# Optimization experiments

Hardware: AMD Instinct MI355X
Metric: run time of the kernel (lower is better)

## Reference

```python
import jax, jax.numpy as jnp
import numpy as np

B, L, D = 1, 2048, 2048
NH, NKV, HD = 32, 8, 64          # heads, kv heads, head_dim = D // NH
THETA = 50000.0
EPS = 1e-5
SCALE = HD ** -0.5


def _rope(x):
    # traditional (interleaved-pair) RoPE; x: (B, H, L, HD)
    hd = x.shape[-1]
    pos = jnp.arange(x.shape[2], dtype=jnp.float32)
    inv = THETA ** (-jnp.arange(0, hd, 2, dtype=jnp.float32) / hd)
    ang = pos[:, None] * inv[None, :]              # (L, HD/2)
    cos, sin = jnp.cos(ang), jnp.sin(ang)
    x1, x2 = x[..., ::2], x[..., 1::2]
    r1 = x1 * cos - x2 * sin
    r2 = x1 * sin + x2 * cos
    return jnp.stack([r1, r2], axis=-1).reshape(x.shape)


def _rmsnorm(x, w):
    return x * jax.lax.rsqrt(jnp.mean(x * x, axis=-1, keepdims=True) + EPS) * w


def setup_inputs() -> dict:
    key = jax.random.key(0)
    ks = jax.random.split(key, 5)
    x = jax.random.normal(ks[0], (B, L, D), dtype=jnp.float32)
    w_qkv = jax.random.normal(ks[1], (NH * HD + 2 * NKV * HD, D), dtype=jnp.float32) * 0.02
    w_out = jax.random.normal(ks[2], (D, D), dtype=jnp.float32) * 0.02
    q_gamma = 1.0 + 0.02 * jax.random.normal(ks[3], (HD,), dtype=jnp.float32)
    k_gamma = 1.0 + 0.02 * jax.random.normal(ks[4], (HD,), dtype=jnp.float32)
    mask = jnp.tril(jnp.ones((L, L), dtype=bool))   # causal
    return {"x": x, "w_qkv": w_qkv, "w_out": w_out,
            "q_gamma": q_gamma, "k_gamma": k_gamma, "mask": mask}


def reference(x, w_qkv, w_out, q_gamma, k_gamma, mask):
    b, l, d = x.shape
    qkv = x @ w_qkv.T                               # fused QKV proj (no bias)
    q, k, v = jnp.split(qkv, [NH * HD, NH * HD + NKV * HD], axis=-1)
    q = q.reshape(b, l, NH, HD).transpose(0, 2, 1, 3)     # (B,NH,L,HD)
    k = k.reshape(b, l, NKV, HD).transpose(0, 2, 1, 3)    # (B,NKV,L,HD)
    v = v.reshape(b, l, NKV, HD).transpose(0, 2, 1, 3)
    q = _rmsnorm(_rope(q), q_gamma)
    k = _rmsnorm(_rope(k), k_gamma)
    g = NH // NKV                                   # GQA group size
    qg = q.reshape(b, NKV, g, l, HD)
    scores = jnp.einsum('bkgqd,bkld->bkgql', qg, k) * SCALE
    scores = jnp.where(mask, scores, -jnp.inf)
    attn = jax.nn.softmax(scores, axis=-1)
    out = jnp.einsum('bkgql,bkld->bkgqd', attn, v)  # (B,NKV,g,L,HD)
    out = out.reshape(b, NH, l, HD).transpose(0, 2, 1, 3).reshape(b, l, d)
    return out @ w_out.T
```

## Files before the change

kernel.cpp:

```cpp
#include <hip/hip_runtime.h>

using bf16   = __bf16;
using bf16x4 = __bf16 __attribute__((ext_vector_type(4)));
using bf16x8 = __bf16 __attribute__((ext_vector_type(8)));
using f32x4  = float __attribute__((ext_vector_type(4)));
using f32x16 = float __attribute__((ext_vector_type(16)));
using u32x2  = unsigned int __attribute__((ext_vector_type(2)));
using u32x4  = unsigned int __attribute__((ext_vector_type(4)));

#define L_SEQ  2048
#define DMODEL 2048
#define NQH    32
#define NKVH   8
#define HDIM   64
#define QKV_N  3072

#define KVF_HSTRIDE (64 * 4 * 64 * 8)

__device__ __forceinline__ void gload_lds16(const void* g, void* lds) {
  __builtin_amdgcn_global_load_lds((__attribute__((address_space(1))) void*)(g),
                                   (__attribute__((address_space(3))) void*)(lds),
                                   16, 0, 0);
}

__device__ __forceinline__ unsigned pack2(float a, float b) {
  union { bf16 h[2]; unsigned u; } x;
  x.h[0] = (bf16)a; x.h[1] = (bf16)b;
  return x.u;
}

__device__ __forceinline__ bf16x8 make_pfrag(float p0, float p1, float p2, float p3,
                                             float p4, float p5, float p6, float p7,
                                             int hi) {
  const unsigned W0 = pack2(p0, p1);
  const unsigned W1 = pack2(p2, p3);
  const unsigned W2 = pack2(p4, p5);
  const unsigned W3 = pack2(p6, p7);
  u32x4 pw;
#if __has_builtin(__builtin_amdgcn_permlane32_swap)
  {
    using i32x2 = int __attribute__((ext_vector_type(2)));
    const i32x2 r02 = __builtin_amdgcn_permlane32_swap((int)W0, (int)W2, false, false);
    const i32x2 r13 = __builtin_amdgcn_permlane32_swap((int)W1, (int)W3, false, false);
    pw = u32x4{ (unsigned)r02[0], (unsigned)r13[0], (unsigned)r02[1], (unsigned)r13[1] };
  }
#else
  {
    const unsigned X0 = (unsigned)__shfl_xor((int)W0, 32);
    const unsigned X1 = (unsigned)__shfl_xor((int)W1, 32);
    const unsigned X2 = (unsigned)__shfl_xor((int)W2, 32);
    const unsigned X3 = (unsigned)__shfl_xor((int)W3, 32);
    pw = u32x4{ hi ? X2 : W0, hi ? X3 : W1, hi ? W2 : X0, hi ? W3 : X1 };
  }
#endif
  return __builtin_bit_cast(bf16x8, pw);
}

__device__ __forceinline__ int chunk_base64(int Qb) {
  return (Qb < 8)  ? Qb
       : (Qb < 16) ? 8  + 2 * (Qb - 8)
       : (Qb < 24) ? 24 + 3 * (Qb - 16)
                   : 48 + 4 * (Qb - 24);
}

#define N4_X  (L_SEQ * DMODEL / 4)
#define N4_WQ (QKV_N * DMODEL / 4)
#define N4_WO (DMODEL * DMODEL / 4)
__global__ void cvt3_f32_bf16(const float* __restrict__ x, const float* __restrict__ wq,
                              const float* __restrict__ wo, bf16* __restrict__ xb,
                              bf16* __restrict__ wqb, bf16* __restrict__ wob) {
  const long stride = (long)gridDim.x * blockDim.x;
  const long ntot = N4_X + N4_WQ + N4_WO;
  for (long i = (long)blockIdx.x * blockDim.x + threadIdx.x; i < ntot; i += stride) {
    const float* src; bf16* dst; long j;
    if (i < N4_X)               { src = x;  dst = xb;  j = i; }
    else if (i < N4_X + N4_WQ)  { src = wq; dst = wqb; j = i - N4_X; }
    else                        { src = wo; dst = wob; j = i - N4_X - N4_WQ; }
    const float4 v = reinterpret_cast<const float4*>(src)[j];
    bf16x4 o = { (bf16)v.x, (bf16)v.y, (bf16)v.z, (bf16)v.w };
    reinterpret_cast<bf16x4*>(dst)[j] = o;
  }
}

template <typename OutT>
__global__ __launch_bounds__(128)
void gemm_bt(const bf16* __restrict__ A, const bf16* __restrict__ B,
             OutT* __restrict__ C, int M, int N, int K) {
  __shared__ bf16 As[128 * 64];
  __shared__ bf16 Bs[64 * 64];
  const int tid = threadIdx.x;
  const int w = tid >> 6, l = tid & 63;
  const int lq = l & 15, lg = l >> 4;
  const long m0 = (long)blockIdx.y * 128;
  const long n0 = (long)blockIdx.x * 64;
  const int ks = K / gridDim.z;
  const int kb = blockIdx.z * ks;
  C += (long)blockIdx.z * M * N;

  const int lrow = l >> 3;
  const int scol = ((l & 7) ^ lrow) << 3;

  f32x4 acc[4][4];
#pragma unroll
  for (int i = 0; i < 4; ++i)
#pragma unroll
    for (int j = 0; j < 4; ++j) acc[i][j] = f32x4{0.f, 0.f, 0.f, 0.f};

  for (int k0 = kb; k0 < kb + ks; k0 += 64) {
#pragma unroll
    for (int i = 0; i < 8; ++i) {
      const int r0 = (i * 2 + w) * 8;
      gload_lds16(A + (m0 + r0 + lrow) * (long)K + k0 + scol, &As[r0 * 64]);
    }
#pragma unroll
    for (int i = 0; i < 4; ++i) {
      const int r0 = (i * 2 + w) * 8;
      gload_lds16(B + (n0 + r0 + lrow) * (long)K + k0 + scol, &Bs[r0 * 64]);
    }
    __syncthreads();
#pragma unroll
    for (int kk = 0; kk < 2; ++kk) {
      bf16x8 af[4], bfr[4];
#pragma unroll
      for (int t = 0; t < 4; ++t) {
        const int rowA = w * 64 + t * 16 + lq;
        const int blkA = (kk * 4 + lg) ^ (rowA & 7);
        af[t] = *reinterpret_cast<const bf16x8*>(&As[rowA * 64 + blkA * 8]);
        const int rowB = t * 16 + lq;
        const int blkB = (kk * 4 + lg) ^ (rowB & 7);
        bfr[t] = *reinterpret_cast<const bf16x8*>(&Bs[rowB * 64 + blkB * 8]);
      }
#pragma unroll
      for (int mt = 0; mt < 4; ++mt)
#pragma unroll
        for (int nt = 0; nt < 4; ++nt)
          acc[mt][nt] = __builtin_amdgcn_mfma_f32_16x16x32_bf16(af[mt], bfr[nt], acc[mt][nt], 0, 0, 0);
    }
    __syncthreads();
  }

#pragma unroll
  for (int mt = 0; mt < 4; ++mt)
#pragma unroll
    for (int r = 0; r < 4; ++r) {
      const long row = m0 + w * 64 + mt * 16 + lg * 4 + r;
#pragma unroll
      for (int nt = 0; nt < 4; ++nt) {
        const long col = n0 + nt * 16 + lq;
        C[row * (long)N + col] = (OutT)acc[mt][nt][r];
      }
    }
}

__global__ __launch_bounds__(256)
void rope_rms(const bf16* __restrict__ pA, const bf16* __restrict__ pB,
              const float* __restrict__ qg, const float* __restrict__ kg,
              bf16* __restrict__ qo, bf16* __restrict__ kfr) {
  const int gid = blockIdx.x * 4 + (threadIdx.x >> 6);
  const int lane = threadIdx.x & 63;
  const int pos = gid / 40;
  const int hh = gid % 40;
  const bool isq = hh < 32;
  const int col = isq ? hh * HDIM : NQH * HDIM + (hh - 32) * HDIM;

  const long idx = (long)pos * QKV_N + col + lane;
  float x = (float)pA[idx] + (float)pB[idx];
  float p = __shfl_xor(x, 1);
  const float fi = (float)(lane & ~1) * (1.0f / 64.0f);
  const float inv = powf(50000.0f, -fi);
  const float ang = (float)pos * inv;
  const float sn = sinf(ang), cs = cosf(ang);
  const float r = (lane & 1) ? (p * sn + x * cs) : (x * cs - p * sn);

  float ss = r * r;
#pragma unroll
  for (int off = 1; off < 64; off <<= 1) ss += __shfl_xor(ss, off);
  const float scl = rsqrtf(ss * (1.0f / 64.0f) + 1e-5f);
  const float g = isq ? qg[lane] : kg[lane];
  const float o = r * scl * g;

  if (isq) {
    qo[(long)pos * DMODEL + hh * HDIM + lane] = (bf16)(o * 0.18033688011112042f);
  } else {
    const int kvh = hh - 32;
    const int d = lane;
    const int lp = (pos & 31) + (((d >> 3) & 1) << 5);
    const long kidx = ((((long)kvh * 64 + (pos >> 5)) * 4 + (d >> 4)) * 64 + lp) * 8 + (d & 7);
    kfr[kidx] = (bf16)o;
  }
}

__global__ __launch_bounds__(256)
void repack_v(const bf16* __restrict__ pA, const bf16* __restrict__ pB,
              bf16* __restrict__ vfr) {
  __shared__ bf16 t[32][72];
  const int kvh = blockIdx.x >> 6;
  const int kb = blockIdx.x & 63;
  const int tid = threadIdx.x;

  {
    const int row = tid >> 3;
    const int cc = (tid & 7) * 8;
    const long goff = (long)(kb * 32 + row) * QKV_N + (NQH * HDIM + NKVH * HDIM) + kvh * HDIM + cc;
    const bf16x8 a = *reinterpret_cast<const bf16x8*>(pA + goff);
    const bf16x8 b = *reinterpret_cast<const bf16x8*>(pB + goff);
    bf16x8 s;
#pragma unroll
    for (int e = 0; e < 8; ++e) s[e] = (bf16)((float)a[e] + (float)b[e]);
    *reinterpret_cast<bf16x8*>(&t[row][cc]) = s;
  }
  __syncthreads();

  const int f = tid >> 6, l = tid & 63;
  const int s = f >> 1, dh = f & 1;
  const int hi = l >> 5, l31 = l & 31;
  union { bf16 b[8]; u32x4 u; } o;
#pragma unroll
  for (int e = 0; e < 8; ++e) o.b[e] = t[s * 16 + hi * 8 + e][dh * 32 + l31];
  bf16* od = vfr + (((long)(kvh * 64 + kb) * 4 + f) * 64 + l) * 8;
  *reinterpret_cast<u32x4*>(od) = o.u;
}

__global__ __launch_bounds__(256, 2)
void flash_attn(const bf16* __restrict__ Q, const bf16* __restrict__ Kfr,
                const bf16* __restrict__ Vfr,
                bf16* __restrict__ po, float* __restrict__ pm, float* __restrict__ pl) {
  const int w = threadIdx.x >> 6, l = threadIdx.x & 63;
  const int lane31 = l & 31, hi = l >> 5;
  const int bb = blockIdx.x;
  const int kvh = bb & 7;
  const int g = 79 - (bb >> 3);

  int Qb, c;
  if (g < 8)       { Qb = g;                   c = 0; }
  else if (g < 24) { Qb = 8 + ((g - 8) >> 1);  c = (g - 8) & 1; }
  else if (g < 48) { Qb = 16 + (g - 24) / 3;   c = (g - 24) % 3; }
  else             { Qb = 24 + ((g - 48) >> 2); c = (g - 48) & 3; }

  const int h = kvh * 4 + w;
  const int s0 = c * 16;
  const int s1 = min(2 * Qb + 2, s0 + 16);
  const int pidx = h * 80 + g;

  const int q0A = Qb * 64;
  const int qA = q0A + lane31;
  const int qB = q0A + 32 + lane31;
  const int l8 = l * 8;

  const bf16* kfrh = Kfr + (long)kvh * KVF_HSTRIDE;
  const bf16* vfrh = Vfr + (long)kvh * KVF_HSTRIDE;

  const bf16* qrowA = Q + (long)qA * DMODEL + h * HDIM + hi * 8;
  const bf16* qrowB = Q + (long)qB * DMODEL + h * HDIM + hi * 8;
  bf16x8 qfA[4], qfB[4];
#pragma unroll
  for (int cc = 0; cc < 4; ++cc) {
    qfA[cc] = *reinterpret_cast<const bf16x8*>(qrowA + cc * 16);
    qfB[cc] = *reinterpret_cast<const bf16x8*>(qrowB + cc * 16);
  }

  f32x16 oA0, oA1, oB0, oB1;
#pragma unroll
  for (int r = 0; r < 16; ++r) { oA0[r] = 0.f; oA1[r] = 0.f; oB0[r] = 0.f; oB1[r] = 0.f; }
  float mA = -3.0e38f, lsA = 0.f, mB = -3.0e38f, lsB = 0.f;

  bf16x8 kc0, kc1, kc2, kc3;
  {
    const bf16* kp = kfrh + (long)s0 * 2048 + l8;
    kc0 = *reinterpret_cast<const bf16x8*>(kp);
    kc1 = *reinterpret_cast<const bf16x8*>(kp + 512);
    kc2 = *reinterpret_cast<const bf16x8*>(kp + 1024);
    kc3 = *reinterpret_cast<const bf16x8*>(kp + 1536);
  }

  for (int sti = s0; sti < s1; ++sti) {
    const int kb0 = sti * 32;

    const bf16* vp = vfrh + (long)sti * 2048 + l8;
    const bf16x8 va0 = *reinterpret_cast<const bf16x8*>(vp);
    const bf16x8 vb0 = *reinterpret_cast<const bf16x8*>(vp + 512);
    const bf16x8 va1 = *reinterpret_cast<const bf16x8*>(vp + 1024);
    const bf16x8 vb1 = *reinterpret_cast<const bf16x8*>(vp + 1536);

    const long knoff = (sti + 1 < s1) ? (long)(sti + 1) * 2048 : (long)s0 * 2048;
    const bf16* kp = kfrh + knoff + l8;
    const bf16x8 kn0 = *reinterpret_cast<const bf16x8*>(kp);
    const bf16x8 kn1 = *reinterpret_cast<const bf16x8*>(kp + 512);
    const bf16x8 kn2 = *reinterpret_cast<const bf16x8*>(kp + 1024);
    const bf16x8 kn3 = *reinterpret_cast<const bf16x8*>(kp + 1536);

    if (kb0 <= q0A + 31) {
      f32x16 st;
#pragma unroll
      for (int r = 0; r < 16; ++r) st[r] = 0.f;
      st = __builtin_amdgcn_mfma_f32_32x32x16_bf16(kc0, qfA[0], st, 0, 0, 0);
      st = __builtin_amdgcn_mfma_f32_32x32x16_bf16(kc1, qfA[1], st, 0, 0, 0);
      st = __builtin_amdgcn_mfma_f32_32x32x16_bf16(kc2, qfA[2], st, 0, 0, 0);
      st = __builtin_amdgcn_mfma_f32_32x32x16_bf16(kc3, qfA[3], st, 0, 0, 0);

      if (kb0 + 31 > q0A) {
#pragma unroll
        for (int r = 0; r < 16; ++r) {
          const int k_abs = kb0 + (r & 3) + 8 * (r >> 2) + 4 * hi;
          if (k_abs > qA) st[r] = -3.0e38f;
        }
      }

      float t[8];
#pragma unroll
      for (int r = 0; r < 8; ++r) t[r] = fmaxf(st[r], st[r + 8]);
#pragma unroll
      for (int s = 4; s > 0; s >>= 1)
#pragma unroll
        for (int r = 0; r < 4; ++r) if (r < s) t[r] = fmaxf(t[r], t[r + s]);
      const float mx = fmaxf(t[0], __shfl_xor(t[0], 32));

      if (!__all(mx - mA <= 8.0f)) {
        const float mn = fmaxf(mA, mx);
        const float al = __builtin_amdgcn_exp2f(mA - mn);
        mA = mn; lsA *= al;
#pragma unroll
        for (int r = 0; r < 16; ++r) { oA0[r] *= al; oA1[r] *= al; }
      }
      float rs = 0.f;
#pragma unroll
      for (int r = 0; r < 16; ++r) { st[r] = __builtin_amdgcn_exp2f(st[r] - mA); rs += st[r]; }
      rs += __shfl_xor(rs, 32);
      lsA += rs;

      const bf16x8 pf0 = make_pfrag(st[0], st[1], st[2], st[3], st[4], st[5], st[6], st[7], hi);
      oA0 = __builtin_amdgcn_mfma_f32_32x32x16_bf16(va0, pf0, oA0, 0, 0, 0);
      oA1 = __builtin_amdgcn_mfma_f32_32x32x16_bf16(vb0, pf0, oA1, 0, 0, 0);
      const bf16x8 pf1 = make_pfrag(st[8], st[9], st[10], st[11], st[12], st[13], st[14], st[15], hi);
      oA0 = __builtin_amdgcn_mfma_f32_32x32x16_bf16(va1, pf1, oA0, 0, 0, 0);
      oA1 = __builtin_amdgcn_mfma_f32_32x32x16_bf16(vb1, pf1, oA1, 0, 0, 0);
    }

    {
      f32x16 st;
#pragma unroll
      for (int r = 0; r < 16; ++r) st[r] = 0.f;
      st = __builtin_amdgcn_mfma_f32_32x32x16_bf16(kc0, qfB[0], st, 0, 0, 0);
      st = __builtin_amdgcn_mfma_f32_32x32x16_bf16(kc1, qfB[1], st, 0, 0, 0);
      st = __builtin_amdgcn_mfma_f32_32x32x16_bf16(kc2, qfB[2], st, 0, 0, 0);
      st = __builtin_amdgcn_mfma_f32_32x32x16_bf16(kc3, qfB[3], st, 0, 0, 0);

      if (kb0 + 31 > q0A + 32) {
#pragma unroll
        for (int r = 0; r < 16; ++r) {
          const int k_abs = kb0 + (r & 3) + 8 * (r >> 2) + 4 * hi;
          if (k_abs > qB) st[r] = -3.0e38f;
        }
      }

      float t[8];
#pragma unroll
      for (int r = 0; r < 8; ++r) t[r] = fmaxf(st[r], st[r + 8]);
#pragma unroll
      for (int s = 4; s > 0; s >>= 1)
#pragma unroll
        for (int r = 0; r < 4; ++r) if (r < s) t[r] = fmaxf(t[r], t[r + s]);
      const float mx = fmaxf(t[0], __shfl_xor(t[0], 32));

      if (!__all(mx - mB <= 8.0f)) {
        const float mn = fmaxf(mB, mx);
        const float al = __builtin_amdgcn_exp2f(mB - mn);
        mB = mn; lsB *= al;
#pragma unroll
        for (int r = 0; r < 16; ++r) { oB0[r] *= al; oB1[r] *= al; }
      }
      float rs = 0.f;
#pragma unroll
      for (int r = 0; r < 16; ++r) { st[r] = __builtin_amdgcn_exp2f(st[r] - mB); rs += st[r]; }
      rs += __shfl_xor(rs, 32);
      lsB += rs;

      const bf16x8 pf0 = make_pfrag(st[0], st[1], st[2], st[3], st[4], st[5], st[6], st[7], hi);
      oB0 = __builtin_amdgcn_mfma_f32_32x32x16_bf16(va0, pf0, oB0, 0, 0, 0);
      oB1 = __builtin_amdgcn_mfma_f32_32x32x16_bf16(vb0, pf0, oB1, 0, 0, 0);
      const bf16x8 pf1 = make_pfrag(st[8], st[9], st[10], st[11], st[12], st[13], st[14], st[15], hi);
      oB0 = __builtin_amdgcn_mfma_f32_32x32x16_bf16(va1, pf1, oB0, 0, 0, 0);
      oB1 = __builtin_amdgcn_mfma_f32_32x32x16_bf16(vb1, pf1, oB1, 0, 0, 0);
    }

    kc0 = kn0; kc1 = kn1; kc2 = kn2; kc3 = kn3;
  }

  bf16* pbase = po + (long)pidx * 4096;
#pragma unroll
  for (int gg = 0; gg < 4; ++gg) {
    const int d0 = 8 * gg + 4 * hi;
    u32x2 a0 = { pack2(oA0[4 * gg + 0], oA0[4 * gg + 1]),
                 pack2(oA0[4 * gg + 2], oA0[4 * gg + 3]) };
    u32x2 a1 = { pack2(oA1[4 * gg + 0], oA1[4 * gg + 1]),
                 pack2(oA1[4 * gg + 2], oA1[4 * gg + 3]) };
    *reinterpret_cast<u32x2*>(pbase + lane31 * 64 + d0) = a0;
    *reinterpret_cast<u32x2*>(pbase + lane31 * 64 + 32 + d0) = a1;
    u32x2 b0 = { pack2(oB0[4 * gg + 0], oB0[4 * gg + 1]),
                 pack2(oB0[4 * gg + 2], oB0[4 * gg + 3]) };
    u32x2 b1 = { pack2(oB1[4 * gg + 0], oB1[4 * gg + 1]),
                 pack2(oB1[4 * gg + 2], oB1[4 * gg + 3]) };
    *reinterpret_cast<u32x2*>(pbase + (32 + lane31) * 64 + d0) = b0;
    *reinterpret_cast<u32x2*>(pbase + (32 + lane31) * 64 + 32 + d0) = b1;
  }
  if (hi == 0) {
    pm[pidx * 64 + lane31] = mA;
    pl[pidx * 64 + lane31] = lsA;
    pm[pidx * 64 + 32 + lane31] = mB;
    pl[pidx * 64 + 32 + lane31] = lsB;
  }
}

__global__ __launch_bounds__(256)
void combine_split(const bf16* __restrict__ po, const float* __restrict__ pm,
                   const float* __restrict__ pl, bf16* __restrict__ ao) {
  const int t = blockIdx.x;
  const int tid = threadIdx.x;
  const int r = tid >> 2;
  const int dc = (tid & 3) * 16;
  const int h = t >> 5, Qb = t & 31;
  const int nc = (Qb < 8) ? 1 : (Qb < 16) ? 2 : (Qb < 24) ? 3 : 4;
  const int p0 = h * 80 + chunk_base64(Qb);

  float mv0 = -3e38f, mv1 = -3e38f, mv2 = -3e38f, mv3 = -3e38f;
  float lv0 = 0.f, lv1 = 0.f, lv2 = 0.f, lv3 = 0.f;
  mv0 = pm[(p0 + 0) * 64 + r];              lv0 = pl[(p0 + 0) * 64 + r];
  if (nc > 1) { mv1 = pm[(p0 + 1) * 64 + r]; lv1 = pl[(p0 + 1) * 64 + r]; }
  if (nc > 2) { mv2 = pm[(p0 + 2) * 64 + r]; lv2 = pl[(p0 + 2) * 64 + r]; }
  if (nc > 3) { mv3 = pm[(p0 + 3) * 64 + r]; lv3 = pl[(p0 + 3) * 64 + r]; }
  const float M = fmaxf(fmaxf(mv0, mv1), fmaxf(mv2, mv3));
  const float w0 = __builtin_amdgcn_exp2f(mv0 - M);
  const float w1 = (nc > 1) ? __builtin_amdgcn_exp2f(mv1 - M) : 0.f;
  const float w2 = (nc > 2) ? __builtin_amdgcn_exp2f(mv2 - M) : 0.f;
  const float w3 = (nc > 3) ? __builtin_amdgcn_exp2f(mv3 - M) : 0.f;
  const float invL = 1.0f / (lv0 * w0 + lv1 * w1 + lv2 * w2 + lv3 * w3);

  float acc[16];
#pragma unroll
  for (int j = 0; j < 16; ++j) acc[j] = 0.f;

#pragma unroll
  for (int c = 0; c < 4; ++c) {
    if (c < nc) {
      const float fc = ((c == 0) ? w0 : (c == 1) ? w1 : (c == 2) ? w2 : w3) * invL;
      const bf16* src = po + ((long)(p0 + c) * 4096) + r * 64 + dc;
      const bf16x8 a0 = *reinterpret_cast<const bf16x8*>(src);
      const bf16x8 a1 = *reinterpret_cast<const bf16x8*>(src + 8);
#pragma unroll
      for (int j = 0; j < 8; ++j) {
        acc[j]     += (float)a0[j] * fc;
        acc[8 + j] += (float)a1[j] * fc;
      }
    }
  }

  const long q_abs = (long)Qb * 64 + r;
  bf16* od = ao + q_abs * DMODEL + h * HDIM + dc;
  union { bf16 b[16]; u32x4 u[2]; } o;
#pragma unroll
  for (int j = 0; j < 16; ++j) o.b[j] = (bf16)acc[j];
  *reinterpret_cast<u32x4*>(od) = o.u[0];
  *reinterpret_cast<u32x4*>(od + 8) = o.u[1];
}

extern "C" void kernel_launch(void* const* d_in, const int* in_sizes, int n_in,
                              void* d_out, int out_size, void* d_ws, size_t ws_size,
                              hipStream_t stream) {
  const float* x       = (const float*)d_in[0];
  const float* w_qkv   = (const float*)d_in[1];
  const float* w_out   = (const float*)d_in[2];
  const float* q_gamma = (const float*)d_in[3];
  const float* k_gamma = (const float*)d_in[4];

  char* ws = (char*)d_ws;
  bf16* xb    = (bf16*)(ws);
  bf16* wqb   = (bf16*)(ws + (8ul  << 20));
  bf16* wob   = (bf16*)(ws + (20ul << 20));
  bf16* qkvpA = (bf16*)(ws + (28ul << 20));
  bf16* qkvpB = (bf16*)(ws + (40ul << 20));
  bf16* qb    = (bf16*)(ws);
  bf16* kfr   = (bf16*)(ws + (8ul  << 20));
  bf16* vfr   = (bf16*)(ws + (10ul << 20));
  bf16* po    = (bf16*)(ws + (28ul << 20));
  float* pm   = (float*)(ws + (48ul << 20));
  float* pl   = (float*)(ws + (49ul << 20));
  bf16* ao    = (bf16*)(ws + (52ul << 20));
  float* out  = (float*)d_out;

  cvt3_f32_bf16<<<2048, 256, 0, stream>>>(x, w_qkv, w_out, xb, wqb, wob);

  gemm_bt<bf16><<<dim3(QKV_N / 64, L_SEQ / 128, 2), 128, 0, stream>>>(xb, wqb, qkvpA, L_SEQ, QKV_N, DMODEL);

  rope_rms<<<(L_SEQ * 40) / 4, 256, 0, stream>>>(qkvpA, qkvpB, q_gamma, k_gamma, qb, kfr);
  repack_v<<<NKVH * (L_SEQ / 32), 256, 0, stream>>>(qkvpA, qkvpB, vfr);

  flash_attn<<<640, 256, 0, stream>>>(qb, kfr, vfr, po, pm, pl);
  combine_split<<<1024, 256, 0, stream>>>(po, pm, pl, ao);

  gemm_bt<float><<<dim3(DMODEL / 64, L_SEQ / 128, 1), 128, 0, stream>>>(ao, wob, out, L_SEQ, DMODEL, DMODEL);
}
```

Baseline: 171.6 us.

## Use fixed softmax offset, drop online max, fuse rope/V repack kernels

Replaces the running-max online softmax in flash attention with a constant exponent offset. This is justified by the RMS-normalised Q and K keeping scores bounded, so the per-tile max reduction, rescaling and the stored max values go away. Split-KV combining becomes a plain sum of partial outputs and row sums. Single-chunk query blocks now write normalised output directly, so combine only runs on multi-chunk blocks. The rope/RMS and V repack kernels are merged into one launch. The risk is overflow or underflow if the gamma weights make scores exceed the assumed bound.

Result: faster. 162.5 us (median of 2 runs) (-5.3%).

```diff
diff --git a/kernel.cpp b/kernel.cpp
--- a/kernel.cpp
+++ b/kernel.cpp
@@ -16,6 +16,8 @@
 #define QKV_N  3072
 
 #define KVF_HSTRIDE (64 * 4 * 64 * 8)
+
+#define FIXED_M 16.0f
 
 __device__ __forceinline__ void gload_lds16(const void* g, void* lds) {
   __builtin_amdgcn_global_load_lds((__attribute__((address_space(1))) void*)(g),
@@ -153,78 +155,76 @@
 }
 
 __global__ __launch_bounds__(256)
-void rope_rms(const bf16* __restrict__ pA, const bf16* __restrict__ pB,
-              const float* __restrict__ qg, const float* __restrict__ kg,
-              bf16* __restrict__ qo, bf16* __restrict__ kfr) {
-  const int gid = blockIdx.x * 4 + (threadIdx.x >> 6);
-  const int lane = threadIdx.x & 63;
-  const int pos = gid / 40;
-  const int hh = gid % 40;
-  const bool isq = hh < 32;
-  const int col = isq ? hh * HDIM : NQH * HDIM + (hh - 32) * HDIM;
-
-  const long idx = (long)pos * QKV_N + col + lane;
-  float x = (float)pA[idx] + (float)pB[idx];
-  float p = __shfl_xor(x, 1);
-  const float fi = (float)(lane & ~1) * (1.0f / 64.0f);
-  const float inv = powf(50000.0f, -fi);
-  const float ang = (float)pos * inv;
-  const float sn = sinf(ang), cs = cosf(ang);
-  const float r = (lane & 1) ? (p * sn + x * cs) : (x * cs - p * sn);
-
-  float ss = r * r;
-#pragma unroll
-  for (int off = 1; off < 64; off <<= 1) ss += __shfl_xor(ss, off);
-  const float scl = rsqrtf(ss * (1.0f / 64.0f) + 1e-5f);
-  const float g = isq ? qg[lane] : kg[lane];
-  const float o = r * scl * g;
-
-  if (isq) {
-    qo[(long)pos * DMODEL + hh * HDIM + lane] = (bf16)(o * 0.18033688011112042f);
+void rope_repack(const bf16* __restrict__ pA, const bf16* __restrict__ pB,
+                 const float* __restrict__ qg, const float* __restrict__ kg,
+                 bf16* __restrict__ qo, bf16* __restrict__ kfr, bf16* __restrict__ vfr) {
+  __shared__ bf16 t[32][72];
+  if (blockIdx.x < 20480) {
+    const int gid = blockIdx.x * 4 + (threadIdx.x >> 6);
+    const int lane = threadIdx.x & 63;
+    const int pos = gid / 40;
+    const int hh = gid % 40;
+    const bool isq = hh < 32;
+    const int col = isq ? hh * HDIM : NQH * HDIM + (hh - 32) * HDIM;
+
+    const long idx = (long)pos * QKV_N + col + lane;
+    float x = (float)pA[idx] + (float)pB[idx];
+    float p = __shfl_xor(x, 1);
+    const float fi = (float)(lane & ~1) * (1.0f / 64.0f);
+    const float inv = powf(50000.0f, -fi);
+    const float ang = (float)pos * inv;
+    const float sn = sinf(ang), cs = cosf(ang);
+    const float r = (lane & 1) ? (p * sn + x * cs) : (x * cs - p * sn);
+
+    float ss = r * r;
+#pragma unroll
+    for (int off = 1; off < 64; off <<= 1) ss += __shfl_xor(ss, off);
+    const float scl = rsqrtf(ss * (1.0f / 64.0f) + 1e-5f);
+    const float g = isq ? qg[lane] : kg[lane];
+    const float o = r * scl * g;
+
+    if (isq) {
+      qo[(long)pos * DMODEL + hh * HDIM + lane] = (bf16)(o * 0.18033688011112042f);
+    } else {
+      const int kvh = hh - 32;
+      const int d = lane;
+      const int lp = (pos & 31) + (((d >> 3) & 1) << 5);
+      const long kidx = ((((long)kvh * 64 + (pos >> 5)) * 4 + (d >> 4)) * 64 + lp) * 8 + (d & 7);
+      kfr[kidx] = (bf16)o;
+    }
   } else {
-    const int kvh = hh - 32;
-    const int d = lane;
-    const int lp = (pos & 31) + (((d >> 3) & 1) << 5);
-    const long kidx = ((((long)kvh * 64 + (pos >> 5)) * 4 + (d >> 4)) * 64 + lp) * 8 + (d & 7);
-    kfr[kidx] = (bf16)o;
-  }
-}
-
-__global__ __launch_bounds__(256)
-void repack_v(const bf16* __restrict__ pA, const bf16* __restrict__ pB,
-              bf16* __restrict__ vfr) {
-  __shared__ bf16 t[32][72];
-  const int kvh = blockIdx.x >> 6;
-  const int kb = blockIdx.x & 63;
-  const int tid = threadIdx.x;
-
-  {
-    const int row = tid >> 3;
-    const int cc = (tid & 7) * 8;
-    const long goff = (long)(kb * 32 + row) * QKV_N + (NQH * HDIM + NKVH * HDIM) + kvh * HDIM + cc;
-    const bf16x8 a = *reinterpret_cast<const bf16x8*>(pA + goff);
-    const bf16x8 b = *reinterpret_cast<const bf16x8*>(pB + goff);
-    bf16x8 s;
-#pragma unroll
-    for (int e = 0; e < 8; ++e) s[e] = (bf16)((float)a[e] + (float)b[e]);
-    *reinterpret_cast<bf16x8*>(&t[row][cc]) = s;
-  }
-  __syncthreads();
-
-  const int f = tid >> 6, l = tid & 63;
-  const int s = f >> 1, dh = f & 1;
-  const int hi = l >> 5, l31 = l & 31;
-  union { bf16 b[8]; u32x4 u; } o;
-#pragma unroll
-  for (int e = 0; e < 8; ++e) o.b[e] = t[s * 16 + hi * 8 + e][dh * 32 + l31];
-  bf16* od = vfr + (((long)(kvh * 64 + kb) * 4 + f) * 64 + l) * 8;
-  *reinterpret_cast<u32x4*>(od) = o.u;
+    const int bid = blockIdx.x - 20480;
+    const int kvh = bid >> 6;
+    const int kb = bid & 63;
+    const int tid = threadIdx.x;
+    {
+      const int row = tid >> 3;
+      const int cc = (tid & 7) * 8;
+      const long goff = (long)(kb * 32 + row) * QKV_N + (NQH * HDIM + NKVH * HDIM) + kvh * HDIM + cc;
+      const bf16x8 a = *reinterpret_cast<const bf16x8*>(pA + goff);
+      const bf16x8 b = *reinterpret_cast<const bf16x8*>(pB + goff);
+      bf16x8 s;
+#pragma unroll
+      for (int e = 0; e < 8; ++e) s[e] = (bf16)((float)a[e] + (float)b[e]);
+      *reinterpret_cast<bf16x8*>(&t[row][cc]) = s;
+    }
+    __syncthreads();
+
+    const int f = tid >> 6, l = tid & 63;
+    const int s = f >> 1, dh = f & 1;
+    const int hi = l >> 5, l31 = l & 31;
+    union { bf16 b[8]; u32x4 u; } o;
+#pragma unroll
+    for (int e = 0; e < 8; ++e) o.b[e] = t[s * 16 + hi * 8 + e][dh * 32 + l31];
+    bf16* od = vfr + (((long)(kvh * 64 + kb) * 4 + f) * 64 + l) * 8;
+    *reinterpret_cast<u32x4*>(od) = o.u;
+  }
 }
 
 __global__ __launch_bounds__(256, 2)
 void flash_attn(const bf16* __restrict__ Q, const bf16* __restrict__ Kfr,
                 const bf16* __restrict__ Vfr,
-                bf16* __restrict__ po, float* __restrict__ pm, float* __restrict__ pl) {
+                bf16* __restrict__ po, float* __restrict__ pl, bf16* __restrict__ ao) {
   const int w = threadIdx.x >> 6, l = threadIdx.x & 63;
   const int lane31 = l & 31, hi = l >> 5;
   const int bb = blockIdx.x;
@@ -262,7 +262,7 @@
   f32x16 oA0, oA1, oB0, oB1;
 #pragma unroll
   for (int r = 0; r < 16; ++r) { oA0[r] = 0.f; oA1[r] = 0.f; oB0[r] = 0.f; oB1[r] = 0.f; }
-  float mA = -3.0e38f, lsA = 0.f, mB = -3.0e38f, lsB = 0.f;
+  float lsA = 0.f, lsB = 0.f;
 
   bf16x8 kc0, kc1, kc2, kc3;
   {
@@ -306,25 +306,9 @@
         }
       }
 
-      float t[8];
-#pragma unroll
-      for (int r = 0; r < 8; ++r) t[r] = fmaxf(st[r], st[r + 8]);
-#pragma unroll
-      for (int s = 4; s > 0; s >>= 1)
-#pragma unroll
-        for (int r = 0; r < 4; ++r) if (r < s) t[r] = fmaxf(t[r], t[r + s]);
-      const float mx = fmaxf(t[0], __shfl_xor(t[0], 32));
-
-      if (!__all(mx - mA <= 8.0f)) {
-        const float mn = fmaxf(mA, mx);
-        const float al = __builtin_amdgcn_exp2f(mA - mn);
-        mA = mn; lsA *= al;
-#pragma unroll
-        for (int r = 0; r < 16; ++r) { oA0[r] *= al; oA1[r] *= al; }
-      }
       float rs = 0.f;
 #pragma unroll
-      for (int r = 0; r < 16; ++r) { st[r] = __builtin_amdgcn_exp2f(st[r] - mA); rs += st[r]; }
+      for (int r = 0; r < 16; ++r) { st[r] = __builtin_amdgcn_exp2f(st[r] - FIXED_M); rs += st[r]; }
       rs += __shfl_xor(rs, 32);
       lsA += rs;
 
@@ -353,25 +337,9 @@
         }
       }
 
-      float t[8];
-#pragma unroll
-      for (int r = 0; r < 8; ++r) t[r] = fmaxf(st[r], st[r + 8]);
-#pragma unroll
-      for (int s = 4; s > 0; s >>= 1)
-#pragma unroll
-        for (int r = 0; r < 4; ++r) if (r < s) t[r] = fmaxf(t[r], t[r + s]);
-      const float mx = fmaxf(t[0], __shfl_xor(t[0], 32));
-
-      if (!__all(mx - mB <= 8.0f)) {
-        const float mn = fmaxf(mB, mx);
-        const float al = __builtin_amdgcn_exp2f(mB - mn);
-        mB = mn; lsB *= al;
-#pragma unroll
-        for (int r = 0; r < 16; ++r) { oB0[r] *= al; oB1[r] *= al; }
-      }
       float rs = 0.f;
 #pragma unroll
-      for (int r = 0; r < 16; ++r) { st[r] = __builtin_amdgcn_exp2f(st[r] - mB); rs += st[r]; }
+      for (int r = 0; r < 16; ++r) { st[r] = __builtin_amdgcn_exp2f(st[r] - FIXED_M); rs += st[r]; }
       rs += __shfl_xor(rs, 32);
       lsB += rs;
 
@@ -386,54 +354,67 @@
     kc0 = kn0; kc1 = kn1; kc2 = kn2; kc3 = kn3;
   }
 
-  bf16* pbase = po + (long)pidx * 4096;
-#pragma unroll
-  for (int gg = 0; gg < 4; ++gg) {
-    const int d0 = 8 * gg + 4 * hi;
-    u32x2 a0 = { pack2(oA0[4 * gg + 0], oA0[4 * gg + 1]),
-                 pack2(oA0[4 * gg + 2], oA0[4 * gg + 3]) };
-    u32x2 a1 = { pack2(oA1[4 * gg + 0], oA1[4 * gg + 1]),
-                 pack2(oA1[4 * gg + 2], oA1[4 * gg + 3]) };
-    *reinterpret_cast<u32x2*>(pbase + lane31 * 64 + d0) = a0;
-    *reinterpret_cast<u32x2*>(pbase + lane31 * 64 + 32 + d0) = a1;
-    u32x2 b0 = { pack2(oB0[4 * gg + 0], oB0[4 * gg + 1]),
-                 pack2(oB0[4 * gg + 2], oB0[4 * gg + 3]) };
-    u32x2 b1 = { pack2(oB1[4 * gg + 0], oB1[4 * gg + 1]),
-                 pack2(oB1[4 * gg + 2], oB1[4 * gg + 3]) };
-    *reinterpret_cast<u32x2*>(pbase + (32 + lane31) * 64 + d0) = b0;
-    *reinterpret_cast<u32x2*>(pbase + (32 + lane31) * 64 + 32 + d0) = b1;
-  }
-  if (hi == 0) {
-    pm[pidx * 64 + lane31] = mA;
-    pl[pidx * 64 + lane31] = lsA;
-    pm[pidx * 64 + 32 + lane31] = mB;
-    pl[pidx * 64 + 32 + lane31] = lsB;
+  if (g < 8) {
+    const float rlA = 1.0f / lsA, rlB = 1.0f / lsB;
+    bf16* orowA = ao + (long)qA * DMODEL + h * HDIM;
+    bf16* orowB = ao + (long)qB * DMODEL + h * HDIM;
+#pragma unroll
+    for (int gg = 0; gg < 4; ++gg) {
+      const int d0 = 8 * gg + 4 * hi;
+      u32x2 a0 = { pack2(oA0[4 * gg + 0] * rlA, oA0[4 * gg + 1] * rlA),
+                   pack2(oA0[4 * gg + 2] * rlA, oA0[4 * gg + 3] * rlA) };
+      u32x2 a1 = { pack2(oA1[4 * gg + 0] * rlA, oA1[4 * gg + 1] * rlA),
+                   pack2(oA1[4 * gg + 2] * rlA, oA1[4 * gg + 3] * rlA) };
+      *reinterpret_cast<u32x2*>(orowA + d0) = a0;
+      *reinterpret_cast<u32x2*>(orowA + 32 + d0) = a1;
+      u32x2 b0 = { pack2(oB0[4 * gg + 0] * rlB, oB0[4 * gg + 1] * rlB),
+                   pack2(oB0[4 * gg + 2] * rlB, oB0[4 * gg + 3] * rlB) };
+      u32x2 b1 = { pack2(oB1[4 * gg + 0] * rlB, oB1[4 * gg + 1] * rlB),
+                   pack2(oB1[4 * gg + 2] * rlB, oB1[4 * gg + 3] * rlB) };
+      *reinterpret_cast<u32x2*>(orowB + d0) = b0;
+      *reinterpret_cast<u32x2*>(orowB + 32 + d0) = b1;
+    }
+  } else {
+    bf16* pbase = po + (long)pidx * 4096;
+#pragma unroll
+    for (int gg = 0; gg < 4; ++gg) {
+      const int d0 = 8 * gg + 4 * hi;
+      u32x2 a0 = { pack2(oA0[4 * gg + 0], oA0[4 * gg + 1]),
+                   pack2(oA0[4 * gg + 2], oA0[4 * gg + 3]) };
+      u32x2 a1 = { pack2(oA1[4 * gg + 0], oA1[4 * gg + 1]),
+                   pack2(oA1[4 * gg + 2], oA1[4 * gg + 3]) };
+      *reinterpret_cast<u32x2*>(pbase + lane31 * 64 + d0) = a0;
+      *reinterpret_cast<u32x2*>(pbase + lane31 * 64 + 32 + d0) = a1;
+      u32x2 b0 = { pack2(oB0[4 * gg + 0], oB0[4 * gg + 1]),
+                   pack2(oB0[4 * gg + 2], oB0[4 * gg + 3]) };
+      u32x2 b1 = { pack2(oB1[4 * gg + 0], oB1[4 * gg + 1]),
+                   pack2(oB1[4 * gg + 2], oB1[4 * gg + 3]) };
+      *reinterpret_cast<u32x2*>(pbase + (32 + lane31) * 64 + d0) = b0;
+      *reinterpret_cast<u32x2*>(pbase + (32 + lane31) * 64 + 32 + d0) = b1;
+    }
+    if (hi == 0) {
+      pl[pidx * 64 + lane31] = lsA;
+      pl[pidx * 64 + 32 + lane31] = lsB;
+    }
   }
 }
 
 __global__ __launch_bounds__(256)
-void combine_split(const bf16* __restrict__ po, const float* __restrict__ pm,
-                   const float* __restrict__ pl, bf16* __restrict__ ao) {
+void combine_split(const bf16* __restrict__ po, const float* __restrict__ pl,
+                   bf16* __restrict__ ao) {
   const int t = blockIdx.x;
   const int tid = threadIdx.x;
   const int r = tid >> 2;
   const int dc = (tid & 3) * 16;
-  const int h = t >> 5, Qb = t & 31;
-  const int nc = (Qb < 8) ? 1 : (Qb < 16) ? 2 : (Qb < 24) ? 3 : 4;
+  const int h = t / 24;
+  const int Qb = 8 + (t % 24);
+  const int nc = (Qb < 16) ? 2 : (Qb < 24) ? 3 : 4;
   const int p0 = h * 80 + chunk_base64(Qb);
 
-  float mv0 = -3e38f, mv1 = -3e38f, mv2 = -3e38f, mv3 = -3e38f;
-  float lv0 = 0.f, lv1 = 0.f, lv2 = 0.f, lv3 = 0.f;
-  mv0 = pm[(p0 + 0) * 64 + r];              lv0 = pl[(p0 + 0) * 64 + r];
-  if (nc > 1) { mv1 = pm[(p0 + 1) * 64 + r]; lv1 = pl[(p0 + 1) * 64 + r]; }
-  if (nc > 2) { mv2 = pm[(p0 + 2) * 64 + r]; lv2 = pl[(p0 + 2) * 64 + r]; }
-  if (nc > 3) { mv3 = pm[(p0 + 3) * 64 + r]; lv3 = pl[(p0 + 3) * 64 + r]; }
-  const float M = fmaxf(fmaxf(mv0, mv1), fmaxf(mv2, mv3));
-  const float w0 = __builtin_amdgcn_exp2f(mv0 - M);
-  const float w1 = (nc > 1) ? __builtin_amdgcn_exp2f(mv1 - M) : 0.f;
-  const float w2 = (nc > 2) ? __builtin_amdgcn_exp2f(mv2 - M) : 0.f;
-  const float w3 = (nc > 3) ? __builtin_amdgcn_exp2f(mv3 - M) : 0.f;
-  const float invL = 1.0f / (lv0 * w0 + lv1 * w1 + lv2 * w2 + lv3 * w3);
+  float lv = pl[(p0 + 0) * 64 + r] + pl[(p0 + 1) * 64 + r];
+  if (nc > 2) lv += pl[(p0 + 2) * 64 + r];
+  if (nc > 3) lv += pl[(p0 + 3) * 64 + r];
+  const float invL = 1.0f / lv;
 
   float acc[16];
 #pragma unroll
@@ -442,14 +423,13 @@
 #pragma unroll
   for (int c = 0; c < 4; ++c) {
     if (c < nc) {
-      const float fc = ((c == 0) ? w0 : (c == 1) ? w1 : (c == 2) ? w2 : w3) * invL;
       const bf16* src = po + ((long)(p0 + c) * 4096) + r * 64 + dc;
       const bf16x8 a0 = *reinterpret_cast<const bf16x8*>(src);
       const bf16x8 a1 = *reinterpret_cast<const bf16x8*>(src + 8);
 #pragma unroll
       for (int j = 0; j < 8; ++j) {
-        acc[j]     += (float)a0[j] * fc;
-        acc[8 + j] += (float)a1[j] * fc;
+        acc[j]     += (float)a0[j];
+        acc[8 + j] += (float)a1[j];
       }
     }
   }
@@ -458,7 +438,7 @@
   bf16* od = ao + q_abs * DMODEL + h * HDIM + dc;
   union { bf16 b[16]; u32x4 u[2]; } o;
 #pragma unroll
-  for (int j = 0; j < 16; ++j) o.b[j] = (bf16)acc[j];
+  for (int j = 0; j < 16; ++j) o.b[j] = (bf16)(acc[j] * invL);
   *reinterpret_cast<u32x4*>(od) = o.u[0];
   *reinterpret_cast<u32x4*>(od + 8) = o.u[1];
 }
@@ -482,8 +462,7 @@
   bf16* kfr   = (bf16*)(ws + (8ul  << 20));
   bf16* vfr   = (bf16*)(ws + (10ul << 20));
   bf16* po    = (bf16*)(ws + (28ul << 20));
-  float* pm   = (float*)(ws + (48ul << 20));
-  float* pl   = (float*)(ws + (49ul << 20));
+  float* pl   = (float*)(ws + (48ul << 20));
   bf16* ao    = (bf16*)(ws + (52ul << 20));
   float* out  = (float*)d_out;
 
@@ -491,11 +470,10 @@
 
   gemm_bt<bf16><<<dim3(QKV_N / 64, L_SEQ / 128, 2), 128, 0, stream>>>(xb, wqb, qkvpA, L_SEQ, QKV_N, DMODEL);
 
-  rope_rms<<<(L_SEQ * 40) / 4, 256, 0, stream>>>(qkvpA, qkvpB, q_gamma, k_gamma, qb, kfr);
-  repack_v<<<NKVH * (L_SEQ / 32), 256, 0, stream>>>(qkvpA, qkvpB, vfr);
-
-  flash_attn<<<640, 256, 0, stream>>>(qb, kfr, vfr, po, pm, pl);
-  combine_split<<<1024, 256, 0, stream>>>(po, pm, pl, ao);
+  rope_repack<<<20992, 256, 0, stream>>>(qkvpA, qkvpB, q_gamma, k_gamma, qb, kfr, vfr);
+
+  flash_attn<<<640, 256, 0, stream>>>(qb, kfr, vfr, po, pl, ao);
+  combine_split<<<768, 256, 0, stream>>>(po, pl, ao);
 
   gemm_bt<float><<<dim3(DMODEL / 64, L_SEQ / 128, 1), 128, 0, stream>>>(ao, wob, out, L_SEQ, DMODEL, DMODEL);
 }
```
